# Kernel optimization log

Hardware: AMD Instinct MI355X
Metric: run time of the kernel (lower is better)

The kernel has to match this reference:

```python
import jax, jax.numpy as jnp
import numpy as np

B, S, D = 4, 2048, 1024  # batch, seq_len, d_emb (even for Givens pairs)


def givens_rotate(r, x):
    """Apply 2x2 Givens block rotations defined by r [D] to x [..., D]."""
    g = r.reshape(-1, 2)
    g = g / jnp.linalg.norm(g, axis=-1, keepdims=True)  # normalize (cos, sin) pairs
    xp = x.reshape(x.shape[:-1] + (x.shape[-1] // 2, 2))
    c, s = g[:, 0], g[:, 1]
    y0 = c * xp[..., 0] - s * xp[..., 1]
    y1 = c * xp[..., 1] + s * xp[..., 0]
    return jnp.stack([y0, y1], axis=-1).reshape(x.shape)


def setup_inputs() -> dict:
    key = jax.random.key(0)
    k1, k2 = jax.random.split(key, 2)
    Q = jax.random.normal(k1, (B, S, D), dtype=jnp.float32)
    # QKV_rotation.weight ~ U(-1, 1) per original init (before the identity overwrite)
    rot_w = jax.random.uniform(k2, (3, D), dtype=jnp.float32, minval=-1.0, maxval=1.0)
    scale = jnp.array([np.sqrt(D)], dtype=jnp.float32)
    bias = jnp.zeros((), dtype=jnp.float32)
    return {"Q": Q, "rot_w": rot_w, "scale": scale, "bias": bias}


def reference(Q, rot_w, scale, bias):
    # Givens-rotation 'projections' for q/k/v
    q = givens_rotate(rot_w[0], Q)
    k = givens_rotate(rot_w[1], Q)
    v = givens_rotate(rot_w[2], Q)
    # prepend zero time coordinate -> points on the Lorentz model ambient space
    zeros = jnp.zeros(Q.shape[:-1] + (1,), Q.dtype)
    q = jnp.concatenate([zeros, q], axis=-1)[:, None]  # [B,1,S,D+1]
    k = jnp.concatenate([zeros, k], axis=-1)[:, None]
    v = jnp.concatenate([zeros, v], axis=-1)[:, None]
    # Lorentz signature (-, +, +, ...)
    sgn = jnp.concatenate([-jnp.ones((1,), Q.dtype), jnp.ones((q.shape[-1] - 1,), Q.dtype)])
    # cinner(q, k): time-negated inner product -> scores [B,1,S,S]
    cin = jnp.einsum('bhqd,bhkd->bhqk', q * sgn, k)
    attn = jax.nn.softmax((2.0 + 2.0 * cin) / scale + bias, axis=-1)
    # Lorentz mid-point: weighted sum normalized by sqrt(|<m,m>_L|)
    ave = jnp.einsum('bhqk,bhkd->bhqd', attn, v)
    inner = jnp.sum(ave * ave * sgn, axis=-1, keepdims=True)
    denom = jnp.sqrt(jnp.clip(jnp.abs(inner), 1e-8, None))
    out = (ave / denom)[:, 0]  # [B,S,D+1]
    return out[..., 1:]  # drop time coordinate -> [B,S,D]
```

## Files before the change

### kernel.cpp

```cpp
#include <hip/hip_runtime.h>

typedef _Float16 h16;
typedef _Float16 half8 __attribute__((ext_vector_type(8)));
typedef _Float16 half4v __attribute__((ext_vector_type(4)));
typedef float floatx4 __attribute__((ext_vector_type(4)));

static constexpr int Bb_ = 4, S_ = 2048, D_ = 1024;

static __device__ __forceinline__ void gl_lds16(const void* g, void* l) {
  __builtin_amdgcn_global_load_lds(
      (const __attribute__((address_space(1))) unsigned int*)g,
      (__attribute__((address_space(3))) unsigned int*)l, 16, 0, 0);
}

__global__ __launch_bounds__(256) void k_prep_t(const float* __restrict__ Q,
                                                const float* __restrict__ rot,
                                                h16* __restrict__ Qh,
                                                h16* __restrict__ Kh,
                                                h16* __restrict__ QhT) {
  __shared__ __align__(16) h16 tile[64][64];
  int d0 = blockIdx.x * 64, s0 = blockIdx.y * 64, b = blockIdx.z;
  int t = threadIdx.x;
  const float* Qb = Q + ((size_t)b * S_ + s0) * D_ + d0;
  h16* Qhb = Qh + ((size_t)b * S_ + s0) * D_ + d0;
  h16* Khb = Kh + ((size_t)b * S_ + s0) * D_ + d0;
#pragma unroll
  for (int i = 0; i < 4; ++i) {
    int c = t + 256 * i;
    int row = c >> 4;
    int col = (c & 15) * 4;
    float4 q = *(const float4*)&Qb[(size_t)row * D_ + col];
    int dg = (d0 + col) >> 2;
    float4 r0 = ((const float4*)rot)[dg];
    float4 r1 = ((const float4*)rot)[D_ / 4 + dg];
    float inq0 = rsqrtf(r0.x * r0.x + r0.y * r0.y);
    float ink0 = rsqrtf(r1.x * r1.x + r1.y * r1.y);
    float cc0 = (r0.x * r1.x + r0.y * r1.y) * inq0 * ink0;
    float ss0 = (r0.x * r1.y - r0.y * r1.x) * inq0 * ink0;
    float y0 = cc0 * q.x - ss0 * q.y;
    float y1 = cc0 * q.y + ss0 * q.x;
    float inq1 = rsqrtf(r0.z * r0.z + r0.w * r0.w);
    float ink1 = rsqrtf(r1.z * r1.z + r1.w * r1.w);
    float cc1 = (r0.z * r1.z + r0.w * r1.w) * inq1 * ink1;
    float ss1 = (r0.z * r1.w - r0.w * r1.z) * inq1 * ink1;
    float y2 = cc1 * q.z - ss1 * q.w;
    float y3 = cc1 * q.w + ss1 * q.z;
    half4v kh = {(h16)y0, (h16)y1, (h16)y2, (h16)y3};
    half4v qh = {(h16)q.x, (h16)q.y, (h16)q.z, (h16)q.w};
    *(half4v*)&Qhb[(size_t)row * D_ + col] = qh;
    *(half4v*)&Khb[(size_t)row * D_ + col] = kh;
    int pcol = col ^ ((row >> 3) << 3);
    *(half4v*)&tile[row][pcol] = qh;
  }
  __syncthreads();
  h16* dst = QhT + ((size_t)b * D_ + d0) * S_ + s0;
#pragma unroll
  for (int i = 0; i < 2; ++i) {
    int c = t + 256 * i;
    int drow = c >> 3;
    int sc = (c & 7) * 8;
    int xr = sc;
    half8 v;
#pragma unroll
    for (int j = 0; j < 8; ++j) v[j] = tile[sc + j][drow ^ xr];
    *(half8*)&dst[(size_t)drow * S_ + sc] = v;
  }
}

template <bool OUT16>
__global__ __launch_bounds__(256) void k_gemm_bt(
    const char* __restrict__ A, int a_pitch, unsigned long long a_batch,
    const char* __restrict__ Bt, int b_pitch, unsigned long long b_batch,
    void* __restrict__ C, int c_pitch, unsigned long long c_batch, int Kdim) {
  __shared__ __align__(16) h16 As[2][128 * 32];
  __shared__ __align__(16) h16 Bs[2][128 * 32];
  const int t = threadIdx.x;
  const int lane = t & 63;
  const int w = t >> 6;
  const int wm = (w >> 1) * 64;
  const int wn = (w & 1) * 64;
  const char* Ab = A + (unsigned long long)blockIdx.z * a_batch +
                   (unsigned long long)blockIdx.y * 128ull * (unsigned long long)a_pitch;
  const char* Bbp = Bt + (unsigned long long)blockIdx.z * b_batch +
                    (unsigned long long)blockIdx.x * 128ull * (unsigned long long)b_pitch;
  const int o0 = t * 16;
  const int o1 = o0 + 4096;
  const int ar0 = o0 >> 6, ar1 = o1 >> 6;
  const int ac0 = ((((o0 >> 4) & 3) ^ ((ar0 >> 1) & 3)) << 4);
  const int ac1 = ((((o1 >> 4) & 3) ^ ((ar1 >> 1) & 3)) << 4);
  const int mrow = lane & 15;
  const int kc = lane >> 4;
  const int koff = ((kc ^ ((mrow >> 1) & 3)) << 3);

  floatx4 acc[4][4];
#pragma unroll
  for (int i = 0; i < 4; ++i)
#pragma unroll
    for (int j = 0; j < 4; ++j) acc[i][j] = (floatx4){0.f, 0.f, 0.f, 0.f};

  for (int kt = 0; kt < Kdim; kt += 64) {
    const int kb = kt * 2;
#pragma unroll
    for (int h = 0; h < 2; ++h) {
      const int hb = kb + h * 64;
      gl_lds16(Ab + (unsigned long long)ar0 * a_pitch + hb + ac0, (char*)As[h] + o0);
      gl_lds16(Ab + (unsigned long long)ar1 * a_pitch + hb + ac1, (char*)As[h] + o1);
      gl_lds16(Bbp + (unsigned long long)ar0 * b_pitch + hb + ac0, (char*)Bs[h] + o0);
      gl_lds16(Bbp + (unsigned long long)ar1 * b_pitch + hb + ac1, (char*)Bs[h] + o1);
    }
    __syncthreads();
#pragma unroll
    for (int h = 0; h < 2; ++h) {
      half8 a[4], b[4];
#pragma unroll
      for (int i = 0; i < 4; ++i)
        a[i] = *(const half8*)&As[h][(wm + i * 16 + mrow) * 32 + koff];
#pragma unroll
      for (int i = 0; i < 4; ++i)
        b[i] = *(const half8*)&Bs[h][(wn + i * 16 + mrow) * 32 + koff];
#pragma unroll
      for (int i = 0; i < 4; ++i)
#pragma unroll
        for (int j = 0; j < 4; ++j)
          acc[i][j] = __builtin_amdgcn_mfma_f32_16x16x32_f16(a[i], b[j], acc[i][j], 0, 0, 0);
    }
    __syncthreads();
  }

  const int m0 = blockIdx.y * 128 + wm;
  const int n0 = blockIdx.x * 128 + wn;
  const int col = lane & 15;
  const int rquad = (lane >> 4) * 4;
  if constexpr (OUT16) {
    h16* Cb = (h16*)C + (unsigned long long)blockIdx.z * c_batch;
#pragma unroll
    for (int i = 0; i < 4; ++i)
#pragma unroll
      for (int j = 0; j < 4; ++j)
#pragma unroll
        for (int r = 0; r < 4; ++r)
          Cb[(unsigned long long)(m0 + i * 16 + rquad + r) * c_pitch + (n0 + j * 16 + col)] =
              (h16)acc[i][j][r];
  } else {
    float* Cb = (float*)C + (unsigned long long)blockIdx.z * c_batch;
#pragma unroll
    for (int i = 0; i < 4; ++i)
#pragma unroll
      for (int j = 0; j < 4; ++j)
#pragma unroll
        for (int r = 0; r < 4; ++r)
          Cb[(unsigned long long)(m0 + i * 16 + rquad + r) * c_pitch + (n0 + j * 16 + col)] =
              acc[i][j][r];
  }
}

__global__ __launch_bounds__(256) void k_softmax(h16* __restrict__ Sl,
                                                 const float* __restrict__ scale_p) {
  int wv = threadIdx.x >> 6, ln = threadIdx.x & 63;
  int row = blockIdx.x * 4 + wv;
  h16* base = Sl + (size_t)row * S_;
  half8 c[4];
#pragma unroll
  for (int r = 0; r < 4; ++r) c[r] = ((const half8*)base)[ln + 64 * r];
  float m = -1e30f;
#pragma unroll
  for (int r = 0; r < 4; ++r)
#pragma unroll
    for (int j = 0; j < 8; ++j) m = fmaxf(m, (float)c[r][j]);
#pragma unroll
  for (int off = 32; off; off >>= 1) m = fmaxf(m, __shfl_xor(m, off));
  float alpha = 2.0f / scale_p[0];
#pragma unroll
  for (int r = 0; r < 4; ++r) {
    half8 pv;
#pragma unroll
    for (int j = 0; j < 8; ++j) pv[j] = (h16)__expf(((float)c[r][j] - m) * alpha);
    ((half8*)base)[ln + 64 * r] = pv;
  }
}

__global__ __launch_bounds__(256) void k_epilogue(float* __restrict__ O,
                                                  const float* __restrict__ rot) {
  int wv = threadIdx.x >> 6, ln = threadIdx.x & 63;
  int row = blockIdx.x * 4 + wv;
  float* base = O + (size_t)row * D_;
  float4 u[4];
#pragma unroll
  for (int r = 0; r < 4; ++r) u[r] = ((const float4*)base)[ln + 64 * r];
  float ss = 0.f;
#pragma unroll
  for (int r = 0; r < 4; ++r)
    ss += u[r].x * u[r].x + u[r].y * u[r].y + u[r].z * u[r].z + u[r].w * u[r].w;
#pragma unroll
  for (int off = 32; off; off >>= 1) ss += __shfl_xor(ss, off);
  float f = rsqrtf(fmaxf(ss, 1e-30f));
#pragma unroll
  for (int r = 0; r < 4; ++r) {
    float4 r2 = ((const float4*)rot)[2 * (D_ / 4) + ln + 64 * r];
    float z0 = u[r].x * f, z1 = u[r].y * f, z2 = u[r].z * f, z3 = u[r].w * f;
    float in0 = rsqrtf(r2.x * r2.x + r2.y * r2.y);
    float cv0 = r2.x * in0, sv0 = r2.y * in0;
    float in1 = rsqrtf(r2.z * r2.z + r2.w * r2.w);
    float cv1 = r2.z * in1, sv1 = r2.w * in1;
    float4 o;
    o.x = cv0 * z0 - sv0 * z1;
    o.y = cv0 * z1 + sv0 * z0;
    o.z = cv1 * z2 - sv1 * z3;
    o.w = cv1 * z3 + sv1 * z2;
    ((float4*)base)[ln + 64 * r] = o;
  }
}

extern "C" void kernel_launch(void* const* d_in, const int* in_sizes, int n_in,
                              void* d_out, int out_size, void* d_ws, size_t ws_size,
                              hipStream_t stream) {
  const float* Q = (const float*)d_in[0];
  const float* rot = (const float*)d_in[1];
  const float* scale = (const float*)d_in[2];
  float* O = (float*)d_out;
  char* ws = (char*)d_ws;
  const size_t MB = 1024ull * 1024ull;
  h16* Qh = (h16*)(ws);
  h16* Kh = (h16*)(ws + 16 * MB);
  h16* QhT = (h16*)(ws + 32 * MB);
  h16* Sl = (h16*)(ws + 48 * MB);

  k_prep_t<<<dim3(D_ / 64, S_ / 64, Bb_), 256, 0, stream>>>(Q, rot, Qh, Kh, QhT);
  k_gemm_bt<true><<<dim3(S_ / 128, S_ / 128, Bb_), 256, 0, stream>>>(
      (const char*)Qh, D_ * 2, (unsigned long long)S_ * D_ * 2,
      (const char*)Kh, D_ * 2, (unsigned long long)S_ * D_ * 2,
      (void*)Sl, S_, (unsigned long long)S_ * S_, D_);
  k_softmax<<<dim3(Bb_ * S_ / 4), 256, 0, stream>>>(Sl, scale);
  k_gemm_bt<false><<<dim3(D_ / 128, S_ / 128, Bb_), 256, 0, stream>>>(
      (const char*)Sl, S_ * 2, (unsigned long long)S_ * S_ * 2,
      (const char*)QhT, S_ * 2, (unsigned long long)D_ * S_ * 2,
      (void*)O, D_, (unsigned long long)S_ * D_, S_);
  k_epilogue<<<dim3(Bb_ * S_ / 4), 256, 0, stream>>>(O, rot);
}
```

Before: 216.4 us.

## Remap GEMM tiles per XCD for L2 locality; pre-rotate V in prep

Block indices in both GEMMs are remapped so that the tiles scheduled on each XCD (selected as id & 7) share A and B panels, which is meant to improve L2 reuse across the chiplets. Separately, the V Givens rotation moves from the epilogue into the prep kernel: the transposed operand is now rotated V instead of raw Q. This makes the epilogue a plain normalisation and relies on the rotation preserving the norm. Prep does slightly more arithmetic per element, and the tile remap hardcodes the grid shapes.

```diff
diff --git a/kernel.cpp b/kernel.cpp
--- a/kernel.cpp
+++ b/kernel.cpp
@@ -17,7 +17,7 @@
                                                 const float* __restrict__ rot,
                                                 h16* __restrict__ Qh,
                                                 h16* __restrict__ Kh,
-                                                h16* __restrict__ QhT) {
+                                                h16* __restrict__ VhT) {
   __shared__ __align__(16) h16 tile[64][64];
   int d0 = blockIdx.x * 64, s0 = blockIdx.y * 64, b = blockIdx.z;
   int t = threadIdx.x;
@@ -33,6 +33,7 @@
     int dg = (d0 + col) >> 2;
     float4 r0 = ((const float4*)rot)[dg];
     float4 r1 = ((const float4*)rot)[D_ / 4 + dg];
+    float4 r2 = ((const float4*)rot)[2 * D_ / 4 + dg];
     float inq0 = rsqrtf(r0.x * r0.x + r0.y * r0.y);
     float ink0 = rsqrtf(r1.x * r1.x + r1.y * r1.y);
     float cc0 = (r0.x * r1.x + r0.y * r1.y) * inq0 * ink0;
@@ -45,15 +46,24 @@
     float ss1 = (r0.z * r1.w - r0.w * r1.z) * inq1 * ink1;
     float y2 = cc1 * q.z - ss1 * q.w;
     float y3 = cc1 * q.w + ss1 * q.z;
+    float inv0 = rsqrtf(r2.x * r2.x + r2.y * r2.y);
+    float cv0 = r2.x * inv0, sv0 = r2.y * inv0;
+    float v0 = cv0 * q.x - sv0 * q.y;
+    float v1 = cv0 * q.y + sv0 * q.x;
+    float inv1 = rsqrtf(r2.z * r2.z + r2.w * r2.w);
+    float cv1 = r2.z * inv1, sv1 = r2.w * inv1;
+    float v2 = cv1 * q.z - sv1 * q.w;
+    float v3 = cv1 * q.w + sv1 * q.z;
     half4v kh = {(h16)y0, (h16)y1, (h16)y2, (h16)y3};
     half4v qh = {(h16)q.x, (h16)q.y, (h16)q.z, (h16)q.w};
+    half4v vh = {(h16)v0, (h16)v1, (h16)v2, (h16)v3};
     *(half4v*)&Qhb[(size_t)row * D_ + col] = qh;
     *(half4v*)&Khb[(size_t)row * D_ + col] = kh;
     int pcol = col ^ ((row >> 3) << 3);
-    *(half4v*)&tile[row][pcol] = qh;
+    *(half4v*)&tile[row][pcol] = vh;
   }
   __syncthreads();
-  h16* dst = QhT + ((size_t)b * D_ + d0) * S_ + s0;
+  h16* dst = VhT + ((size_t)b * D_ + d0) * S_ + s0;
 #pragma unroll
   for (int i = 0; i < 2; ++i) {
     int c = t + 256 * i;
@@ -79,10 +89,27 @@
   const int w = t >> 6;
   const int wm = (w >> 1) * 64;
   const int wn = (w & 1) * 64;
-  const char* Ab = A + (unsigned long long)blockIdx.z * a_batch +
-                   (unsigned long long)blockIdx.y * 128ull * (unsigned long long)a_pitch;
-  const char* Bbp = Bt + (unsigned long long)blockIdx.z * b_batch +
-                    (unsigned long long)blockIdx.x * 128ull * (unsigned long long)b_pitch;
+
+  const int id = blockIdx.x + gridDim.x * (blockIdx.y + 16 * blockIdx.z);
+  const int xcd = id & 7;
+  const int s = id >> 3;
+  int tm, tn, tz;
+  if constexpr (OUT16) {
+    tz = s >> 5;
+    int tt = s & 31;
+    tm = (xcd >> 1) * 4 + (tt >> 3);
+    tn = (xcd & 1) * 8 + (tt & 7);
+  } else {
+    tz = s >> 4;
+    int tt = s & 15;
+    tm = (xcd >> 1) * 4 + (tt >> 2);
+    tn = (xcd & 1) * 4 + (tt & 3);
+  }
+
+  const char* Ab = A + (unsigned long long)tz * a_batch +
+                   (unsigned long long)tm * 128ull * (unsigned long long)a_pitch;
+  const char* Bbp = Bt + (unsigned long long)tz * b_batch +
+                    (unsigned long long)tn * 128ull * (unsigned long long)b_pitch;
   const int o0 = t * 16;
   const int o1 = o0 + 4096;
   const int ar0 = o0 >> 6, ar1 = o1 >> 6;
@@ -127,12 +154,12 @@
     __syncthreads();
   }
 
-  const int m0 = blockIdx.y * 128 + wm;
-  const int n0 = blockIdx.x * 128 + wn;
+  const int m0 = tm * 128 + wm;
+  const int n0 = tn * 128 + wn;
   const int col = lane & 15;
   const int rquad = (lane >> 4) * 4;
   if constexpr (OUT16) {
-    h16* Cb = (h16*)C + (unsigned long long)blockIdx.z * c_batch;
+    h16* Cb = (h16*)C + (unsigned long long)tz * c_batch;
 #pragma unroll
     for (int i = 0; i < 4; ++i)
 #pragma unroll
@@ -142,7 +169,7 @@
           Cb[(unsigned long long)(m0 + i * 16 + rquad + r) * c_pitch + (n0 + j * 16 + col)] =
               (h16)acc[i][j][r];
   } else {
-    float* Cb = (float*)C + (unsigned long long)blockIdx.z * c_batch;
+    float* Cb = (float*)C + (unsigned long long)tz * c_batch;
 #pragma unroll
     for (int i = 0; i < 4; ++i)
 #pragma unroll
@@ -179,8 +206,7 @@
   }
 }
 
-__global__ __launch_bounds__(256) void k_epilogue(float* __restrict__ O,
-                                                  const float* __restrict__ rot) {
+__global__ __launch_bounds__(256) void k_epilogue(float* __restrict__ O) {
   int wv = threadIdx.x >> 6, ln = threadIdx.x & 63;
   int row = blockIdx.x * 4 + wv;
   float* base = O + (size_t)row * D_;
@@ -196,17 +222,11 @@
   float f = rsqrtf(fmaxf(ss, 1e-30f));
 #pragma unroll
   for (int r = 0; r < 4; ++r) {
-    float4 r2 = ((const float4*)rot)[2 * (D_ / 4) + ln + 64 * r];
-    float z0 = u[r].x * f, z1 = u[r].y * f, z2 = u[r].z * f, z3 = u[r].w * f;
-    float in0 = rsqrtf(r2.x * r2.x + r2.y * r2.y);
-    float cv0 = r2.x * in0, sv0 = r2.y * in0;
-    float in1 = rsqrtf(r2.z * r2.z + r2.w * r2.w);
-    float cv1 = r2.z * in1, sv1 = r2.w * in1;
     float4 o;
-    o.x = cv0 * z0 - sv0 * z1;
-    o.y = cv0 * z1 + sv0 * z0;
-    o.z = cv1 * z2 - sv1 * z3;
-    o.w = cv1 * z3 + sv1 * z2;
+    o.x = u[r].x * f;
+    o.y = u[r].y * f;
+    o.z = u[r].z * f;
+    o.w = u[r].w * f;
     ((float4*)base)[ln + 64 * r] = o;
   }
 }
@@ -222,10 +242,10 @@
   const size_t MB = 1024ull * 1024ull;
   h16* Qh = (h16*)(ws);
   h16* Kh = (h16*)(ws + 16 * MB);
-  h16* QhT = (h16*)(ws + 32 * MB);
+  h16* VhT = (h16*)(ws + 32 * MB);
   h16* Sl = (h16*)(ws + 48 * MB);
 
-  k_prep_t<<<dim3(D_ / 64, S_ / 64, Bb_), 256, 0, stream>>>(Q, rot, Qh, Kh, QhT);
+  k_prep_t<<<dim3(D_ / 64, S_ / 64, Bb_), 256, 0, stream>>>(Q, rot, Qh, Kh, VhT);
   k_gemm_bt<true><<<dim3(S_ / 128, S_ / 128, Bb_), 256, 0, stream>>>(
       (const char*)Qh, D_ * 2, (unsigned long long)S_ * D_ * 2,
       (const char*)Kh, D_ * 2, (unsigned long long)S_ * D_ * 2,
@@ -233,7 +253,7 @@
   k_softmax<<<dim3(Bb_ * S_ / 4), 256, 0, stream>>>(Sl, scale);
   k_gemm_bt<false><<<dim3(D_ / 128, S_ / 128, Bb_), 256, 0, stream>>>(
       (const char*)Sl, S_ * 2, (unsigned long long)S_ * S_ * 2,
-      (const char*)QhT, S_ * 2, (unsigned long long)D_ * S_ * 2,
+      (const char*)VhT, S_ * 2, (unsigned long long)D_ * S_ * 2,
       (void*)O, D_, (unsigned long long)S_ * D_, S_);
-  k_epilogue<<<dim3(Bb_ * S_ / 4), 256, 0, stream>>>(O, rot);
-}
+  k_epilogue<<<dim3(Bb_ * S_ / 4), 256, 0, stream>>>(O);
+}
```

Result: faster. 208.7 us (-3.6%).
